# Kernel optimization log

Measured on AMD Instinct MI355X. Metric: run time of the kernel, lower is better.

Reference implementation:

```python
import jax, jax.numpy as jnp
import numpy as np

B, S, D, H, DK, DV = 4, 1024, 1024, 16, 64, 64
NEG = -1e9  # matches torch masked_fill(-1000000000.0)


def setup_inputs() -> dict:
    key = jax.random.key(0)
    ks = jax.random.split(key, 12)
    scale = 1.0 / np.sqrt(D)
    return {
        "querys": jax.random.normal(ks[0], (B, S, D), jnp.float32),
        "keys": jax.random.normal(ks[1], (B, S, D), jnp.float32),
        "values": jax.random.normal(ks[2], (B, S, D), jnp.float32),
        "mask": jax.random.randint(ks[3], (S, S), 0, 2, jnp.int32),
        # stacked per-head projection params (nn.Linear style: y = x @ W^T + b -> here W stored as [D, dk])
        "Wq": jax.random.normal(ks[4], (H, D, DK), jnp.float32) * scale,
        "bq": jax.random.normal(ks[5], (H, DK), jnp.float32) * 0.01,
        "Wk": jax.random.normal(ks[6], (H, D, DK), jnp.float32) * scale,
        "bk": jax.random.normal(ks[7], (H, DK), jnp.float32) * 0.01,
        "Wv": jax.random.normal(ks[8], (H, D, DV), jnp.float32) * scale,
        "bv": jax.random.normal(ks[9], (H, DV), jnp.float32) * 0.01,
        "Wp": jax.random.normal(ks[10], (H * DV, D), jnp.float32) * (1.0 / np.sqrt(H * DV)),
        "bp": jax.random.normal(ks[11], (D,), jnp.float32) * 0.01,
    }


def reference(querys, keys, values, mask, Wq, bq, Wk, bk, Wv, bv, Wp, bp):
    # per-head projections, all heads batched: [B, H, S, dk/dv]
    q = jnp.einsum('bsd,hdk->bhsk', querys, Wq) + bq[None, :, None, :]
    k = jnp.einsum('bsd,hdk->bhsk', keys, Wk) + bk[None, :, None, :]
    v = jnp.einsum('bsd,hdv->bhsv', values, Wv) + bv[None, :, None, :]
    # scores: NO 1/sqrt(dk) scaling, faithful to original broadcast multiply+sum
    scores = jnp.einsum('bhqd,bhkd->bhqk', q, k)  # [B, H, S, S]
    scores = jnp.where(mask[None, None, :, :] == 0, NEG, scores)
    w = jax.nn.softmax(scores, axis=-1)
    o = jnp.einsum('bhqk,bhkv->bhqv', w, v)        # [B, H, S, dv]
    # concat heads along feature dim (head order = H axis), then project
    o = o.transpose(0, 2, 1, 3).reshape(B, S, H * DV)
    return o @ Wp + bp
```

## Files before the change

kernel.cpp:

```cpp
#include <hip/hip_runtime.h>
#include <hip/hip_bf16.h>

typedef unsigned short u16;
typedef unsigned long long u64;
typedef __attribute__((ext_vector_type(4))) float f32x4;
typedef __attribute__((ext_vector_type(8))) __bf16 bf16x8;
typedef __attribute__((ext_vector_type(8))) u16 u16x8;
typedef __attribute__((ext_vector_type(4))) u16 u16x4;

#define DEV __device__ __forceinline__
#define MFMA(a, b, c) __builtin_amdgcn_mfma_f32_16x16x32_bf16(a, b, c, 0, 0, 0)


DEV u16 f2bf(float x) {
  unsigned u = __builtin_bit_cast(unsigned, x);
  u += 0x7fffu + ((u >> 16) & 1u);
  return (u16)(u >> 16);
}
DEV float bf2f(u16 h) {
  unsigned u = ((unsigned)h) << 16;
  return __builtin_bit_cast(float, u);
}
DEV bf16x8 frag8(const u16* p) {
  return __builtin_bit_cast(bf16x8, *(const u16x8*)p);
}

__global__ __launch_bounds__(256) void prep_weights(
    const float* __restrict__ Wq, const float* __restrict__ Wk,
    const float* __restrict__ Wv, const float* __restrict__ Wp,
    u16* __restrict__ wqh, u16* __restrict__ wql,
    u16* __restrict__ wkh, u16* __restrict__ wkl,
    u16* __restrict__ wvh, u16* __restrict__ wph) {
  __shared__ float tile[64][65];
  const int k0 = blockIdx.x * 64;
  const int h = blockIdx.y;
  const int z = blockIdx.z;
  const float* src;
  u16* dhi;
  u16* dlo = nullptr;
  int hs, rs;
  if (z == 0)      { src = Wq; dhi = wqh; dlo = wql; hs = 65536; rs = 64; }
  else if (z == 1) { src = Wk; dhi = wkh; dlo = wkl; hs = 65536; rs = 64; }
  else if (z == 2) { src = Wv; dhi = wvh;            hs = 65536; rs = 64; }
  else             { src = Wp; dhi = wph;            hs = 64;    rs = 1024; }
  const int t = threadIdx.x;
#pragma unroll
  for (int i = 0; i < 16; ++i) {
    int kk = i * 4 + (t >> 6), nn = t & 63;
    tile[kk][nn] = src[h * hs + (k0 + kk) * rs + nn];
  }
  __syncthreads();
#pragma unroll
  for (int i = 0; i < 16; ++i) {
    int nn = i * 4 + (t >> 6), kk = t & 63;
    float x = tile[kk][nn];
    u16 hi = f2bf(x);
    int idx = (h * 64 + nn) * 1024 + k0 + kk;
    dhi[idx] = hi;
    if (dlo) dlo[idx] = f2bf(x - bf2f(hi));
  }
}

__global__ __launch_bounds__(256) void pack_mask(const int* __restrict__ mask,
                                                 u64* __restrict__ mp) {
  int g = blockIdx.x * 4 + (threadIdx.x >> 6);
  int lane = threadIdx.x & 63;
  int v = mask[(g >> 4) * 1024 + (g & 15) * 64 + lane];
  u64 bits = __ballot(v != 0);
  if (lane == 0) mp[g] = bits;
}

__global__ __launch_bounds__(256, 3) void proj_fused(
    const float* __restrict__ Xq, const float* __restrict__ Xk,
    const float* __restrict__ Xv, const u16* __restrict__ wqh,
    const u16* __restrict__ wql, const u16* __restrict__ wkh,
    const u16* __restrict__ wkl, const u16* __restrict__ wvh,
    const float* __restrict__ bq, const float* __restrict__ bk,
    const float* __restrict__ bv, u16* __restrict__ Qh, u16* __restrict__ Ql,
    u16* __restrict__ Kh, u16* __restrict__ Kl, u16* __restrict__ Vt) {
  __shared__ alignas(16) u16 Ah[128 * 48];
  __shared__ alignas(16) u16 Al[128 * 48];
  __shared__ alignas(16) u16 Bh[128 * 48];
  __shared__ alignas(16) u16 Bl[128 * 48];
  const int z = blockIdx.z;
  const bool split = (z < 2);
  const float* X = (z == 0) ? Xq : (z == 1) ? Xk : Xv;
  const u16* Bth = (z == 0) ? wqh : (z == 1) ? wkh : wvh;
  const u16* Btl = (z == 0) ? wql : wkl;
  const float* bias = (z == 0) ? bq : (z == 1) ? bk : bv;
  u16* Oh = (z == 0) ? Qh : (z == 1) ? Kh : Vt;
  u16* Ol = (z == 0) ? Ql : Kl;

  const int m0 = blockIdx.x * 128, n0 = blockIdx.y * 128;
  const int t = threadIdx.x, w = t >> 6, l = t & 63;
  const int wr = w >> 1, wc = w & 1, lr = l & 15, lq = l >> 4;
  f32x4 acc[4][4];
#pragma unroll
  for (int i = 0; i < 4; ++i)
#pragma unroll
    for (int j = 0; j < 4; ++j) acc[i][j] = (f32x4){0.f, 0.f, 0.f, 0.f};

  for (int ks = 0; ks < 32; ++ks) {
    const int k0 = ks * 32;
#pragma unroll
    for (int i = 0; i < 4; ++i) {
      int r = (t >> 3) + i * 32, c = (t & 7) * 4;
      f32x4 v = *(const f32x4*)&X[(m0 + r) * 1024 + k0 + c];
      u16x4 hi, lo;
#pragma unroll
      for (int e = 0; e < 4; ++e) {
        u16 hh = f2bf(v[e]);
        hi[e] = hh;
        lo[e] = f2bf(v[e] - bf2f(hh));
      }
      *(u16x4*)&Ah[r * 48 + c] = hi;
      if (split) *(u16x4*)&Al[r * 48 + c] = lo;
    }
#pragma unroll
    for (int i = 0; i < 2; ++i) {
      int r = (t >> 2) + i * 64, c = (t & 3) * 8;
      *(u16x8*)&Bh[r * 48 + c] = *(const u16x8*)&Bth[(n0 + r) * 1024 + k0 + c];
      if (split)
        *(u16x8*)&Bl[r * 48 + c] = *(const u16x8*)&Btl[(n0 + r) * 1024 + k0 + c];
    }
    __syncthreads();
    bf16x8 ah[4], al[4];
#pragma unroll
    for (int mi = 0; mi < 4; ++mi) {
      int row = wr * 64 + mi * 16 + lr;
      ah[mi] = frag8(&Ah[row * 48 + lq * 8]);
      if (split) al[mi] = frag8(&Al[row * 48 + lq * 8]);
    }
    if (split) {
#pragma unroll
      for (int nj = 0; nj < 4; ++nj) {
        int col = wc * 64 + nj * 16 + lr;
        bf16x8 bh = frag8(&Bh[col * 48 + lq * 8]);
        bf16x8 bl = frag8(&Bl[col * 48 + lq * 8]);
#pragma unroll
        for (int mi = 0; mi < 4; ++mi) {
          acc[mi][nj] = MFMA(ah[mi], bh, acc[mi][nj]);
          acc[mi][nj] = MFMA(ah[mi], bl, acc[mi][nj]);
          acc[mi][nj] = MFMA(al[mi], bh, acc[mi][nj]);
        }
      }
    } else {
#pragma unroll
      for (int nj = 0; nj < 4; ++nj) {
        int col = wc * 64 + nj * 16 + lr;
        bf16x8 bh = frag8(&Bh[col * 48 + lq * 8]);
#pragma unroll
        for (int mi = 0; mi < 4; ++mi) acc[mi][nj] = MFMA(ah[mi], bh, acc[mi][nj]);
      }
    }
    __syncthreads();
  }
#pragma unroll
  for (int nj = 0; nj < 4; ++nj) {
    int n = n0 + wc * 64 + nj * 16 + lr;
    float bb = bias[n];
    int h = n >> 6, dk = n & 63;
#pragma unroll
    for (int mi = 0; mi < 4; ++mi) {
#pragma unroll
      for (int j = 0; j < 4; ++j) {
        int m = m0 + wr * 64 + mi * 16 + lq * 4 + j;
        int b = m >> 10, s = m & 1023;
        float x = acc[mi][nj][j] + bb;
        if (split) {
          int idx = ((b * 16 + h) * 1024 + s) * 64 + dk;
          u16 hh = f2bf(x);
          Oh[idx] = hh;
          Ol[idx] = f2bf(x - bf2f(hh));
        } else {
          int idx = ((b * 16 + h) * 64 + dk) * 1024 + s;
          Oh[idx] = f2bf(x);
        }
      }
    }
  }
}

__global__ __launch_bounds__(256, 4) void attn_kernel(
    const u16* __restrict__ Qh, const u16* __restrict__ Ql,
    const u16* __restrict__ Kh, const u16* __restrict__ Kl,
    const u16* __restrict__ Vt, const u64* __restrict__ mp,
    u16* __restrict__ Oc) {
  __shared__ alignas(16) u16 Ks_h[64 * 72];
  __shared__ alignas(16) u16 Ks_l[64 * 72];
  __shared__ alignas(16) u16 Vs[64 * 72];
  __shared__ alignas(16) u16 Ps[4][16 * 72];
  __shared__ u64 mw[64];
  const int bid = blockIdx.x;
  const int bh = bid >> 4, qt = bid & 15, q0 = qt * 64;
  const int t = threadIdx.x, w = t >> 6, l = t & 63;
  const int lr = l & 15, lq = l >> 4;
  const int qrow = q0 + w * 16 + lr;
  const int rr = t >> 2, c0 = (t & 3) * 8;

  bf16x8 qh[2], qlo[2];
#pragma unroll
  for (int d = 0; d < 2; ++d) {
    int off = (bh * 1024 + qrow) * 64 + d * 32 + lq * 8;
    qh[d] = frag8(&Qh[off]);
    qlo[d] = frag8(&Ql[off]);
  }
  f32x4 o[4];
#pragma unroll
  for (int dv = 0; dv < 4; ++dv) o[dv] = (f32x4){0.f, 0.f, 0.f, 0.f};
  float mr[4] = {-1e30f, -1e30f, -1e30f, -1e30f};
  float lsum[4] = {0.f, 0.f, 0.f, 0.f};

  u16x8 rKh[2], rKl[2], rVs[2];
  u64 rMw = 0;
  auto issue = [&](int kt) {
    const int k0 = kt * 64;
#pragma unroll
    for (int half = 0; half < 2; ++half) {
      int c = c0 + half * 32;
      rKh[half] = *(const u16x8*)&Kh[(bh * 1024 + k0 + rr) * 64 + c];
      rKl[half] = *(const u16x8*)&Kl[(bh * 1024 + k0 + rr) * 64 + c];
      rVs[half] = *(const u16x8*)&Vt[(bh * 64 + rr) * 1024 + k0 + c];
    }
    if (t < 64) rMw = mp[(q0 + t) * 16 + kt];
  };

  issue(0);
  for (int kt = 0; kt < 16; ++kt) {
#pragma unroll
    for (int half = 0; half < 2; ++half) {
      int c = c0 + half * 32;
      *(u16x8*)&Ks_h[rr * 72 + c] = rKh[half];
      *(u16x8*)&Ks_l[rr * 72 + c] = rKl[half];
      *(u16x8*)&Vs[rr * 72 + c] = rVs[half];
    }
    if (t < 64) mw[t] = rMw;
    __syncthreads();
    if (kt < 15) issue(kt + 1);
    f32x4 s[4];
#pragma unroll
    for (int kb = 0; kb < 4; ++kb) {
      f32x4 a = (f32x4){0.f, 0.f, 0.f, 0.f};
#pragma unroll
      for (int d = 0; d < 2; ++d) {
        bf16x8 kfh = frag8(&Ks_h[(kb * 16 + lr) * 72 + d * 32 + lq * 8]);
        bf16x8 kfl = frag8(&Ks_l[(kb * 16 + lr) * 72 + d * 32 + lq * 8]);
        a = MFMA(qh[d], kfh, a);
        a = MFMA(qh[d], kfl, a);
        a = MFMA(qlo[d], kfh, a);
      }
      s[kb] = a;
    }
#pragma unroll
    for (int j = 0; j < 4; ++j) {
      u64 word = mw[w * 16 + lq * 4 + j];
      float mx = -3e38f;
#pragma unroll
      for (int kb = 0; kb < 4; ++kb) {
        float v = s[kb][j];
        if (!((word >> (kb * 16 + lr)) & 1ull)) v = -1e9f;
        s[kb][j] = v;
        mx = fmaxf(mx, v);
      }
#pragma unroll
      for (int mk = 1; mk < 16; mk <<= 1) mx = fmaxf(mx, __shfl_xor(mx, mk));
      float mn = fmaxf(mr[j], mx);
      float scale = __expf(mr[j] - mn);
      mr[j] = mn;
      float ps = 0.f;
#pragma unroll
      for (int kb = 0; kb < 4; ++kb) {
        float p = __expf(s[kb][j] - mn);
        s[kb][j] = p;
        ps += p;
      }
#pragma unroll
      for (int mk = 1; mk < 16; mk <<= 1) ps += __shfl_xor(ps, mk);
      lsum[j] = lsum[j] * scale + ps;
#pragma unroll
      for (int dv = 0; dv < 4; ++dv) o[dv][j] *= scale;
    }
    u16* pw = &Ps[w][0];
#pragma unroll
    for (int j = 0; j < 4; ++j)
#pragma unroll
      for (int kb = 0; kb < 4; ++kb)
        pw[(lq * 4 + j) * 72 + kb * 16 + lr] = f2bf(s[kb][j]);
#pragma unroll
    for (int kk = 0; kk < 2; ++kk) {
      bf16x8 pa = frag8(&pw[lr * 72 + kk * 32 + lq * 8]);
#pragma unroll
      for (int dv = 0; dv < 4; ++dv) {
        bf16x8 vf = frag8(&Vs[(dv * 16 + lr) * 72 + kk * 32 + lq * 8]);
        o[dv] = MFMA(pa, vf, o[dv]);
      }
    }
    __syncthreads();
  }
  const int b = bh >> 4, h = bh & 15;
#pragma unroll
  for (int j = 0; j < 4; ++j) {
    float inv = 1.f / lsum[j];
    int srow = q0 + w * 16 + lq * 4 + j;
    int base = (b * 1024 + srow) * 1024 + h * 64;
#pragma unroll
    for (int dv = 0; dv < 4; ++dv) Oc[base + dv * 16 + lr] = f2bf(o[dv][j] * inv);
  }
}

__global__ __launch_bounds__(256) void final_kernel(
    const u16* __restrict__ A, const u16* __restrict__ Bt,
    const float* __restrict__ bias, float* __restrict__ out) {
  __shared__ alignas(16) u16 As[64 * 48];
  __shared__ alignas(16) u16 Bs[128 * 48];
  const int m0 = blockIdx.x * 64, n0 = blockIdx.y * 128;
  const int t = threadIdx.x, w = t >> 6, l = t & 63;
  const int wr = w >> 1, wc = w & 1, lr = l & 15, lq = l >> 4;
  f32x4 acc[2][4];
#pragma unroll
  for (int i = 0; i < 2; ++i)
#pragma unroll
    for (int j = 0; j < 4; ++j) acc[i][j] = (f32x4){0.f, 0.f, 0.f, 0.f};

  for (int ks = 0; ks < 32; ++ks) {
    int k0 = ks * 32;
    {
      int r = t >> 2, c = (t & 3) * 8;
      *(u16x8*)&As[r * 48 + c] = *(const u16x8*)&A[(m0 + r) * 1024 + k0 + c];
#pragma unroll
      for (int i = 0; i < 2; ++i) {
        int rb = r + i * 64;
        *(u16x8*)&Bs[rb * 48 + c] = *(const u16x8*)&Bt[(n0 + rb) * 1024 + k0 + c];
      }
    }
    __syncthreads();
    bf16x8 a[2];
#pragma unroll
    for (int mi = 0; mi < 2; ++mi)
      a[mi] = frag8(&As[(wr * 32 + mi * 16 + lr) * 48 + lq * 8]);
#pragma unroll
    for (int nj = 0; nj < 4; ++nj) {
      bf16x8 bfr = frag8(&Bs[(wc * 64 + nj * 16 + lr) * 48 + lq * 8]);
#pragma unroll
      for (int mi = 0; mi < 2; ++mi) acc[mi][nj] = MFMA(a[mi], bfr, acc[mi][nj]);
    }
    __syncthreads();
  }
#pragma unroll
  for (int nj = 0; nj < 4; ++nj) {
    int n = n0 + wc * 64 + nj * 16 + lr;
    float bb = bias[n];
#pragma unroll
    for (int mi = 0; mi < 2; ++mi)
#pragma unroll
      for (int j = 0; j < 4; ++j) {
        int m = m0 + wr * 32 + mi * 16 + lq * 4 + j;
        out[m * 1024 + n] = acc[mi][nj][j] + bb;
      }
  }
}

extern "C" void kernel_launch(void* const* d_in, const int* in_sizes, int n_in,
                              void* d_out, int out_size, void* d_ws, size_t ws_size,
                              hipStream_t stream) {
  (void)in_sizes; (void)n_in; (void)out_size; (void)ws_size;
  const float* querys = (const float*)d_in[0];
  const float* keys = (const float*)d_in[1];
  const float* values = (const float*)d_in[2];
  const int* mask = (const int*)d_in[3];
  const float* Wq = (const float*)d_in[4];
  const float* bq = (const float*)d_in[5];
  const float* Wk = (const float*)d_in[6];
  const float* bk = (const float*)d_in[7];
  const float* Wv = (const float*)d_in[8];
  const float* bv = (const float*)d_in[9];
  const float* Wp = (const float*)d_in[10];
  const float* bp = (const float*)d_in[11];
  float* out = (float*)d_out;

  char* ws = (char*)d_ws;
  const size_t MB = 1024ull * 1024ull;
  u16* Qh = (u16*)(ws + 0 * MB);
  u16* Ql = (u16*)(ws + 8 * MB);
  u16* Kh = (u16*)(ws + 16 * MB);
  u16* Kl = (u16*)(ws + 24 * MB);
  u16* Vt = (u16*)(ws + 32 * MB);
  u16* Oc = (u16*)(ws + 40 * MB);
  u16* wqh = (u16*)(ws + 48 * MB);
  u16* wql = (u16*)(ws + 50 * MB);
  u16* wkh = (u16*)(ws + 52 * MB);
  u16* wkl = (u16*)(ws + 54 * MB);
  u16* wvh = (u16*)(ws + 56 * MB);
  u16* wph = (u16*)(ws + 58 * MB);
  u64* mp = (u64*)(ws + 60 * MB);

  prep_weights<<<dim3(16, 16, 4), 256, 0, stream>>>(Wq, Wk, Wv, Wp, wqh, wql, wkh,
                                                    wkl, wvh, wph);
  pack_mask<<<dim3(4096), 256, 0, stream>>>(mask, mp);
  proj_fused<<<dim3(32, 8, 3), 256, 0, stream>>>(querys, keys, values, wqh, wql,
                                                 wkh, wkl, wvh, bq, bk, bv, Qh, Ql,
                                                 Kh, Kl, Vt);
  attn_kernel<<<dim3(1024), 256, 0, stream>>>(Qh, Ql, Kh, Kl, Vt, mp, Oc);
  final_kernel<<<dim3(64, 8), 256, 0, stream>>>(Oc, wph, bp, out);
}
```

Before: 370.2 us.

## Pre-split inputs to bf16 and stage GEMM tiles via direct global-to-LDS loads

```diff
diff --git a/kernel.cpp b/kernel.cpp
--- a/kernel.cpp
+++ b/kernel.cpp
@@ -6,7 +6,6 @@
 typedef __attribute__((ext_vector_type(4))) float f32x4;
 typedef __attribute__((ext_vector_type(8))) __bf16 bf16x8;
 typedef __attribute__((ext_vector_type(8))) u16 u16x8;
-typedef __attribute__((ext_vector_type(4))) u16 u16x4;
 
 #define DEV __device__ __forceinline__
 #define MFMA(a, b, c) __builtin_amdgcn_mfma_f32_16x16x32_bf16(a, b, c, 0, 0, 0)
@@ -23,6 +22,10 @@
 }
 DEV bf16x8 frag8(const u16* p) {
   return __builtin_bit_cast(bf16x8, *(const u16x8*)p);
+}
+DEV void gload16(u16* lds, const u16* g) {
+  __builtin_amdgcn_global_load_lds((const __attribute__((address_space(1))) void*)g,
+                                   (__attribute__((address_space(3))) void*)lds, 16, 0, 0);
 }
 
 __global__ __launch_bounds__(256) void prep_weights(
@@ -70,23 +73,50 @@
   if (lane == 0) mp[g] = bits;
 }
 
-__global__ __launch_bounds__(256, 3) void proj_fused(
-    const float* __restrict__ Xq, const float* __restrict__ Xk,
-    const float* __restrict__ Xv, const u16* __restrict__ wqh,
+__global__ __launch_bounds__(256) void split_x(
+    const float* __restrict__ q, const float* __restrict__ k,
+    const float* __restrict__ v, u16* __restrict__ qh, u16* __restrict__ ql,
+    u16* __restrict__ kh, u16* __restrict__ kl, u16* __restrict__ vh) {
+  const int z = blockIdx.y;
+  const float* src = (z == 0) ? q : (z == 1) ? k : v;
+  u16* dh = (z == 0) ? qh : (z == 1) ? kh : vh;
+  u16* dl = (z == 0) ? ql : kl;
+  const bool split = (z < 2);
+  const long base = (long)(blockIdx.x * 256 + threadIdx.x) * 8;
+  f32x4 v0 = *(const f32x4*)&src[base];
+  f32x4 v1 = *(const f32x4*)&src[base + 4];
+  u16x8 hi, lo;
+#pragma unroll
+  for (int e = 0; e < 4; ++e) {
+    u16 h0 = f2bf(v0[e]), h1 = f2bf(v1[e]);
+    hi[e] = h0;
+    hi[4 + e] = h1;
+    lo[e] = f2bf(v0[e] - bf2f(h0));
+    lo[4 + e] = f2bf(v1[e] - bf2f(h1));
+  }
+  *(u16x8*)&dh[base] = hi;
+  if (split) *(u16x8*)&dl[base] = lo;
+}
+
+__global__ __launch_bounds__(256, 4) void proj_fused(
+    const u16* __restrict__ Xqh, const u16* __restrict__ Xql,
+    const u16* __restrict__ Xkh, const u16* __restrict__ Xkl,
+    const u16* __restrict__ Xvh, const u16* __restrict__ wqh,
     const u16* __restrict__ wql, const u16* __restrict__ wkh,
     const u16* __restrict__ wkl, const u16* __restrict__ wvh,
     const float* __restrict__ bq, const float* __restrict__ bk,
     const float* __restrict__ bv, u16* __restrict__ Qh, u16* __restrict__ Ql,
     u16* __restrict__ Kh, u16* __restrict__ Kl, u16* __restrict__ Vt) {
-  __shared__ alignas(16) u16 Ah[128 * 48];
-  __shared__ alignas(16) u16 Al[128 * 48];
-  __shared__ alignas(16) u16 Bh[128 * 48];
-  __shared__ alignas(16) u16 Bl[128 * 48];
+  __shared__ alignas(16) u16 Ah[128 * 32];
+  __shared__ alignas(16) u16 Al[128 * 32];
+  __shared__ alignas(16) u16 Bh[128 * 32];
+  __shared__ alignas(16) u16 Bl[128 * 32];
   const int z = blockIdx.z;
   const bool split = (z < 2);
-  const float* X = (z == 0) ? Xq : (z == 1) ? Xk : Xv;
-  const u16* Bth = (z == 0) ? wqh : (z == 1) ? wkh : wvh;
-  const u16* Btl = (z == 0) ? wql : wkl;
+  const u16* Ah_src = (z == 0) ? Xqh : (z == 1) ? Xkh : Xvh;
+  const u16* Al_src = (z == 0) ? Xql : Xkl;
+  const u16* Bh_src = (z == 0) ? wqh : (z == 1) ? wkh : wvh;
+  const u16* Bl_src = (z == 0) ? wql : wkl;
   const float* bias = (z == 0) ? bq : (z == 1) ? bk : bv;
   u16* Oh = (z == 0) ? Qh : (z == 1) ? Kh : Vt;
   u16* Ol = (z == 0) ? Ql : Kl;
@@ -94,6 +124,7 @@
   const int m0 = blockIdx.x * 128, n0 = blockIdx.y * 128;
   const int t = threadIdx.x, w = t >> 6, l = t & 63;
   const int wr = w >> 1, wc = w & 1, lr = l & 15, lq = l >> 4;
+  const int srow = l >> 2, scol = (l & 3) * 8;
   f32x4 acc[4][4];
 #pragma unroll
   for (int i = 0; i < 4; ++i)
@@ -103,40 +134,30 @@
   for (int ks = 0; ks < 32; ++ks) {
     const int k0 = ks * 32;
 #pragma unroll
-    for (int i = 0; i < 4; ++i) {
-      int r = (t >> 3) + i * 32, c = (t & 7) * 4;
-      f32x4 v = *(const f32x4*)&X[(m0 + r) * 1024 + k0 + c];
-      u16x4 hi, lo;
-#pragma unroll
-      for (int e = 0; e < 4; ++e) {
-        u16 hh = f2bf(v[e]);
-        hi[e] = hh;
-        lo[e] = f2bf(v[e] - bf2f(hh));
-      }
-      *(u16x4*)&Ah[r * 48 + c] = hi;
-      if (split) *(u16x4*)&Al[r * 48 + c] = lo;
-    }
-#pragma unroll
     for (int i = 0; i < 2; ++i) {
-      int r = (t >> 2) + i * 64, c = (t & 3) * 8;
-      *(u16x8*)&Bh[r * 48 + c] = *(const u16x8*)&Bth[(n0 + r) * 1024 + k0 + c];
-      if (split)
-        *(u16x8*)&Bl[r * 48 + c] = *(const u16x8*)&Btl[(n0 + r) * 1024 + k0 + c];
+      const int ci = w * 2 + i;
+      const int rr = ci * 16 + srow;
+      gload16(&Ah[ci * 512], &Ah_src[(m0 + rr) * 1024 + k0 + scol]);
+      gload16(&Bh[ci * 512], &Bh_src[(n0 + rr) * 1024 + k0 + scol]);
+      if (split) {
+        gload16(&Al[ci * 512], &Al_src[(m0 + rr) * 1024 + k0 + scol]);
+        gload16(&Bl[ci * 512], &Bl_src[(n0 + rr) * 1024 + k0 + scol]);
+      }
     }
     __syncthreads();
     bf16x8 ah[4], al[4];
 #pragma unroll
     for (int mi = 0; mi < 4; ++mi) {
       int row = wr * 64 + mi * 16 + lr;
-      ah[mi] = frag8(&Ah[row * 48 + lq * 8]);
-      if (split) al[mi] = frag8(&Al[row * 48 + lq * 8]);
+      ah[mi] = frag8(&Ah[row * 32 + lq * 8]);
+      if (split) al[mi] = frag8(&Al[row * 32 + lq * 8]);
     }
     if (split) {
 #pragma unroll
       for (int nj = 0; nj < 4; ++nj) {
         int col = wc * 64 + nj * 16 + lr;
-        bf16x8 bh = frag8(&Bh[col * 48 + lq * 8]);
-        bf16x8 bl = frag8(&Bl[col * 48 + lq * 8]);
+        bf16x8 bh = frag8(&Bh[col * 32 + lq * 8]);
+        bf16x8 bl = frag8(&Bl[col * 32 + lq * 8]);
 #pragma unroll
         for (int mi = 0; mi < 4; ++mi) {
           acc[mi][nj] = MFMA(ah[mi], bh, acc[mi][nj]);
@@ -148,7 +169,7 @@
 #pragma unroll
       for (int nj = 0; nj < 4; ++nj) {
         int col = wc * 64 + nj * 16 + lr;
-        bf16x8 bh = frag8(&Bh[col * 48 + lq * 8]);
+        bf16x8 bh = frag8(&Bh[col * 32 + lq * 8]);
 #pragma unroll
         for (int mi = 0; mi < 4; ++mi) acc[mi][nj] = MFMA(ah[mi], bh, acc[mi][nj]);
       }
@@ -311,11 +332,12 @@
 __global__ __launch_bounds__(256) void final_kernel(
     const u16* __restrict__ A, const u16* __restrict__ Bt,
     const float* __restrict__ bias, float* __restrict__ out) {
-  __shared__ alignas(16) u16 As[64 * 48];
-  __shared__ alignas(16) u16 Bs[128 * 48];
+  __shared__ alignas(16) u16 As[64 * 32];
+  __shared__ alignas(16) u16 Bs[128 * 32];
   const int m0 = blockIdx.x * 64, n0 = blockIdx.y * 128;
   const int t = threadIdx.x, w = t >> 6, l = t & 63;
   const int wr = w >> 1, wc = w & 1, lr = l & 15, lq = l >> 4;
+  const int srow = l >> 2, scol = (l & 3) * 8;
   f32x4 acc[2][4];
 #pragma unroll
   for (int i = 0; i < 2; ++i)
@@ -323,24 +345,21 @@
     for (int j = 0; j < 4; ++j) acc[i][j] = (f32x4){0.f, 0.f, 0.f, 0.f};
 
   for (int ks = 0; ks < 32; ++ks) {
-    int k0 = ks * 32;
-    {
-      int r = t >> 2, c = (t & 3) * 8;
-      *(u16x8*)&As[r * 48 + c] = *(const u16x8*)&A[(m0 + r) * 1024 + k0 + c];
-#pragma unroll
-      for (int i = 0; i < 2; ++i) {
-        int rb = r + i * 64;
-        *(u16x8*)&Bs[rb * 48 + c] = *(const u16x8*)&Bt[(n0 + rb) * 1024 + k0 + c];
-      }
+    const int k0 = ks * 32;
+    gload16(&As[w * 512], &A[(m0 + w * 16 + srow) * 1024 + k0 + scol]);
+#pragma unroll
+    for (int i = 0; i < 2; ++i) {
+      const int ci = w * 2 + i;
+      gload16(&Bs[ci * 512], &Bt[(n0 + ci * 16 + srow) * 1024 + k0 + scol]);
     }
     __syncthreads();
     bf16x8 a[2];
 #pragma unroll
     for (int mi = 0; mi < 2; ++mi)
-      a[mi] = frag8(&As[(wr * 32 + mi * 16 + lr) * 48 + lq * 8]);
+      a[mi] = frag8(&As[(wr * 32 + mi * 16 + lr) * 32 + lq * 8]);
 #pragma unroll
     for (int nj = 0; nj < 4; ++nj) {
-      bf16x8 bfr = frag8(&Bs[(wc * 64 + nj * 16 + lr) * 48 + lq * 8]);
+      bf16x8 bfr = frag8(&Bs[(wc * 64 + nj * 16 + lr) * 32 + lq * 8]);
 #pragma unroll
       for (int mi = 0; mi < 2; ++mi) acc[mi][nj] = MFMA(a[mi], bfr, acc[mi][nj]);
     }
@@ -392,12 +411,19 @@
   u16* wkl = (u16*)(ws + 54 * MB);
   u16* wvh = (u16*)(ws + 56 * MB);
   u16* wph = (u16*)(ws + 58 * MB);
-  u64* mp = (u64*)(ws + 60 * MB);
+  u16* Xkl = (u16*)(ws + 60 * MB);
+  u16* Xvh = (u16*)(ws + 68 * MB);
+  u64* mp = (u64*)(ws + 76 * MB);
+  u16* Xqh = (u16*)d_out;
+  u16* Xql = (u16*)((char*)d_out + 8 * MB);
+  u16* Xkh = Oc;
 
   prep_weights<<<dim3(16, 16, 4), 256, 0, stream>>>(Wq, Wk, Wv, Wp, wqh, wql, wkh,
                                                     wkl, wvh, wph);
   pack_mask<<<dim3(4096), 256, 0, stream>>>(mask, mp);
-  proj_fused<<<dim3(32, 8, 3), 256, 0, stream>>>(querys, keys, values, wqh, wql,
+  split_x<<<dim3(2048, 3), 256, 0, stream>>>(querys, keys, values, Xqh, Xql, Xkh,
+                                             Xkl, Xvh);
+  proj_fused<<<dim3(32, 8, 3), 256, 0, stream>>>(Xqh, Xql, Xkh, Xkl, Xvh, wqh, wql,
                                                  wkh, wkl, wvh, bq, bk, bv, Qh, Ql,
                                                  Kh, Kl, Vt);
   attn_kernel<<<dim3(1024), 256, 0, stream>>>(Qh, Ql, Kh, Kl, Vt, mp, Oc);
```

After: 531.8 us. 1.44x slower.
